# Performance work log

Hardware: AMD Instinct MI355X
Metric: run time of the kernel (lower is better)

## Reference

```python
import jax, jax.numpy as jnp
import numpy as np

N_NODES = 100000
N_EDGES = 3200000
N_GRAPHS = 1000
IN_C, HID_C, OUT_C = 128, 128, 10
BN_EPS = 1e-5


def setup_inputs() -> dict:
    key = jax.random.key(0)
    ks = jax.random.split(key, 16)
    s = lambda k, shape, fan: jax.random.normal(k, shape, jnp.float32) * (1.0 / np.sqrt(fan))
    x = jax.random.normal(ks[0], (N_NODES, IN_C), jnp.float32)
    edge_index = jax.random.randint(ks[1], (2, N_EDGES), 0, N_NODES, dtype=jnp.int64)
    batch = jnp.sort(jax.random.randint(ks[2], (N_NODES,), 0, N_GRAPHS, dtype=jnp.int64))
    return {
        "x": x, "edge_index": edge_index, "batch": batch,
        "W1a": s(ks[3], (IN_C, HID_C), IN_C), "b1a": jnp.zeros((HID_C,), jnp.float32),
        "W1b": s(ks[4], (HID_C, HID_C), HID_C), "b1b": jnp.zeros((HID_C,), jnp.float32),
        "g1": jnp.ones((HID_C,), jnp.float32), "be1": jnp.zeros((HID_C,), jnp.float32),
        "W2a": s(ks[5], (HID_C, HID_C), HID_C), "b2a": jnp.zeros((HID_C,), jnp.float32),
        "W2b": s(ks[6], (HID_C, HID_C), HID_C), "b2b": jnp.zeros((HID_C,), jnp.float32),
        "g2": jnp.ones((HID_C,), jnp.float32), "be2": jnp.zeros((HID_C,), jnp.float32),
        "Wlin": s(ks[7], (HID_C, OUT_C), HID_C), "blin": jnp.zeros((OUT_C,), jnp.float32),
    }


def _batchnorm(h, gamma, beta):
    # BatchNorm1d, training mode: batch statistics (biased variance, as torch)
    mean = jnp.mean(h, axis=0)
    var = jnp.mean(jnp.square(h - mean), axis=0)
    return (h - mean) * jax.lax.rsqrt(var + BN_EPS) * gamma + beta


def _gin_conv(x, src, dst, Wa, ba, Wb, bb, gamma, beta):
    # GINConv with eps=0: mlp(x + sum_{j->i} x_j); scatter-add over dst
    agg = jax.ops.segment_sum(x[src], dst, num_segments=N_NODES)
    h = x + agg
    h = jax.nn.relu(h @ Wa + ba) @ Wb + bb
    return _batchnorm(h, gamma, beta)


def reference(x, edge_index, batch, W1a, b1a, W1b, b1b, g1, be1,
              W2a, b2a, W2b, b2b, g2, be2, Wlin, blin):
    src, dst = edge_index[0], edge_index[1]
    h = jax.nn.relu(_gin_conv(x, src, dst, W1a, b1a, W1b, b1b, g1, be1))
    h = jax.nn.relu(_gin_conv(h, src, dst, W2a, b2a, W2b, b2b, g2, be2))
    pooled = jax.ops.segment_sum(h, batch, num_segments=N_GRAPHS)  # [G, HID_C]
    logits = pooled @ Wlin + blin
    return jax.nn.log_softmax(logits, axis=1)
```

## Files before the change

### kernel.cpp

```cpp
#include <hip/hip_runtime.h>
#include <hip/hip_bf16.h>

#define NN 100000
#define NE 3200000
#define NG 1000
#define BN_EPS 1e-5f

#define BKT_SH 6
#define BKTN 64
#define NBKT 1563
#define CHUNK 8192
#define NBINBLK 391
#define BNBLK 512

typedef __attribute__((ext_vector_type(8))) short short8v;
typedef __attribute__((ext_vector_type(4))) float f32x4;

__device__ __forceinline__ unsigned int f2bf(float f) {
    unsigned int u = __builtin_bit_cast(unsigned int, f);
    u += 0x7FFFu + ((u >> 16) & 1u);
    return u >> 16;
}
__device__ __forceinline__ float bf2f(unsigned int h16) {
    return __builtin_bit_cast(float, h16 << 16);
}

__global__ __launch_bounds__(256) void bucket_count_kernel(const int* __restrict__ dst,
                                                           int* __restrict__ bcnt) {
    __shared__ int h[NBKT];
    int t = threadIdx.x;
    for (int i = t; i < NBKT; i += 256) h[i] = 0;
    __syncthreads();
    int gid = blockIdx.x * 256 + t;
    for (int e = gid; e < NE; e += NBINBLK * 256) atomicAdd(&h[dst[e] >> BKT_SH], 1);
    __syncthreads();
    for (int i = t; i < NBKT; i += 256) if (h[i]) atomicAdd(&bcnt[i], h[i]);
}

__global__ void bucket_scan_kernel(const int* __restrict__ bcnt, int* __restrict__ bbase,
                                   int* __restrict__ bcur) {
    __shared__ int wsum[16];
    __shared__ int lcarry;
    int t = threadIdx.x, lane = t & 63, w = t >> 6;
    if (t == 0) lcarry = 0;
    __syncthreads();
    for (int base = 0; base < NBKT; base += 1024) {
        int i = base + t;
        int v = (i < NBKT) ? bcnt[i] : 0;
        int incl = v;
        #pragma unroll
        for (int d = 1; d < 64; d <<= 1) { int u = __shfl_up(incl, d, 64); if (lane >= d) incl += u; }
        if (lane == 63) wsum[w] = incl;
        __syncthreads();
        if (w == 0) {
            int s = (lane < 16) ? wsum[lane] : 0;
            #pragma unroll
            for (int d = 1; d < 16; d <<= 1) { int u = __shfl_up(s, d, 64); if (lane >= d) s += u; }
            if (lane < 16) wsum[lane] = s;
        }
        __syncthreads();
        int excl = lcarry + (w ? wsum[w - 1] : 0) + incl - v;
        if (i < NBKT) { bbase[i] = excl; bcur[i] = excl; }
        __syncthreads();
        if (t == 0) lcarry += wsum[15];
        __syncthreads();
    }
}

__global__ __launch_bounds__(256) void bin_kernel(const int* __restrict__ src,
        const int* __restrict__ dst, int* __restrict__ bcur,
        unsigned int* __restrict__ ebin) {
    __shared__ unsigned int ebuf[CHUNK];
    __shared__ unsigned short bids[CHUNK];
    __shared__ int hist[NBKT], lbase[NBKT], lcur[NBKT], delta[NBKT];
    __shared__ int wsum4[4];
    __shared__ int carry;
    int t = threadIdx.x;
    int lane = t & 63, w = t >> 6;
    int c0 = blockIdx.x * CHUNK;
    int cnt = min(CHUNK, NE - c0);
    for (int i = t; i < NBKT; i += 256) hist[i] = 0;
    if (t == 0) carry = 0;
    __syncthreads();
    for (int i = t; i < cnt; i += 256) atomicAdd(&hist[dst[c0 + i] >> BKT_SH], 1);
    __syncthreads();
    for (int bb = 0; bb < NBKT; bb += 256) {
        int i = bb + t;
        int v = (i < NBKT) ? hist[i] : 0;
        int incl = v;
        #pragma unroll
        for (int d2 = 1; d2 < 64; d2 <<= 1) { int u = __shfl_up(incl, d2, 64); if (lane >= d2) incl += u; }
        if (lane == 63) wsum4[w] = incl;
        __syncthreads();
        int wo = 0;
        if (w > 0) wo = wsum4[0];
        if (w > 1) wo += wsum4[1];
        if (w > 2) wo += wsum4[2];
        int excl = carry + wo + incl - v;
        if (i < NBKT) { lbase[i] = excl; lcur[i] = excl; }
        int tot = wsum4[0] + wsum4[1] + wsum4[2] + wsum4[3];
        __syncthreads();
        if (t == 0) carry += tot;
        __syncthreads();
    }
    for (int b = t; b < NBKT; b += 256) {
        int hh = hist[b];
        delta[b] = (hh ? atomicAdd(&bcur[b], hh) : 0) - lbase[b];
    }
    __syncthreads();
    for (int i = t; i < cnt; i += 256) {
        int d = dst[c0 + i];
        int s = src[c0 + i];
        int b = d >> BKT_SH;
        unsigned int entry = ((unsigned int)s << BKT_SH) | (unsigned int)(d & (BKTN - 1));
        int p = atomicAdd(&lcur[b], 1);
        ebuf[p] = entry;
        bids[p] = (unsigned short)b;
    }
    __syncthreads();
    for (int i = t; i < cnt; i += 256) {
        ebin[delta[bids[i]] + i] = ebuf[i];
    }
}

__global__ __launch_bounds__(256) void sort_kernel(const unsigned int* __restrict__ ebin,
        const int* __restrict__ bbase, const int* __restrict__ bcnt,
        int* __restrict__ noffs, int* __restrict__ csrc) {
    __shared__ int nh[BKTN], ncur[BKTN];
    int b = blockIdx.x, t = threadIdx.x;
    int base = bbase[b], cnt = bcnt[b];
    if (t < BKTN) nh[t] = 0;
    __syncthreads();
    for (int i = t; i < cnt; i += 256) atomicAdd(&nh[ebin[base + i] & (BKTN - 1)], 1);
    __syncthreads();
    if (t < 64) {
        int v = nh[t], incl = v;
        #pragma unroll
        for (int d = 1; d < 64; d <<= 1) { int u = __shfl_up(incl, d, 64); if (t >= d) incl += u; }
        int excl = incl - v;
        ncur[t] = excl;
        int node = (b << BKT_SH) + t;
        if (node < NN) noffs[node] = base + excl;
    }
    if (b == 0 && t == 0) noffs[NN] = NE;
    __syncthreads();
    for (int i = t; i < cnt; i += 256) {
        unsigned int e = ebin[base + i];
        int p = atomicAdd(&ncur[e & (BKTN - 1)], 1);
        csrc[base + p] = (int)(e >> BKT_SH);
    }
}

__global__ void pack_x_kernel(const float* __restrict__ x, unsigned int* __restrict__ xp) {
    int tid = blockIdx.x * 256 + threadIdx.x;
    float2 v = ((const float2*)x)[tid];
    xp[tid] = f2bf(v.x) | (f2bf(v.y) << 16);
}

__global__ void wprep_kernel(const float* __restrict__ W1a, const float* __restrict__ W1b,
                             const float* __restrict__ W2a, const float* __restrict__ W2b,
                             unsigned int* __restrict__ Wt) {
    int tid = blockIdx.x * 256 + threadIdx.x;
    int m = tid >> 13;
    int r = tid & 8191;
    int c = r >> 6, kh = r & 63;
    const float* W = (m == 0) ? W1a : (m == 1) ? W1b : (m == 2) ? W2a : W2b;
    float a = W[(2 * kh) * 128 + c];
    float b = W[(2 * kh + 1) * 128 + c];
    Wt[tid] = f2bf(a) | (f2bf(b) << 16);
}

__global__ __launch_bounds__(256) void aggregate_gather_kernel(
        const unsigned int* __restrict__ xp, const int* __restrict__ noffs,
        const int* __restrict__ csrc, unsigned int* __restrict__ outp) {
    int node = __builtin_amdgcn_readfirstlane(blockIdx.x * 4 + (threadIdx.x >> 6));
    int lane = threadIdx.x & 63;
    unsigned int u = xp[(size_t)node * 64 + lane];
    float alo = bf2f(u & 0xFFFFu), ahi = bf2f(u >> 16);
    int s = noffs[node], e = noffs[node + 1];
    int i = s;
    for (; i + 8 <= e; i += 8) {
        int i0 = csrc[i + 0], i1 = csrc[i + 1], i2 = csrc[i + 2], i3 = csrc[i + 3];
        int i4 = csrc[i + 4], i5 = csrc[i + 5], i6 = csrc[i + 6], i7 = csrc[i + 7];
        unsigned int u0 = xp[(size_t)i0 * 64 + lane];
        unsigned int u1 = xp[(size_t)i1 * 64 + lane];
        unsigned int u2 = xp[(size_t)i2 * 64 + lane];
        unsigned int u3 = xp[(size_t)i3 * 64 + lane];
        unsigned int u4 = xp[(size_t)i4 * 64 + lane];
        unsigned int u5 = xp[(size_t)i5 * 64 + lane];
        unsigned int u6 = xp[(size_t)i6 * 64 + lane];
        unsigned int u7 = xp[(size_t)i7 * 64 + lane];
        alo += bf2f(u0 & 0xFFFFu); ahi += bf2f(u0 >> 16);
        alo += bf2f(u1 & 0xFFFFu); ahi += bf2f(u1 >> 16);
        alo += bf2f(u2 & 0xFFFFu); ahi += bf2f(u2 >> 16);
        alo += bf2f(u3 & 0xFFFFu); ahi += bf2f(u3 >> 16);
        alo += bf2f(u4 & 0xFFFFu); ahi += bf2f(u4 >> 16);
        alo += bf2f(u5 & 0xFFFFu); ahi += bf2f(u5 >> 16);
        alo += bf2f(u6 & 0xFFFFu); ahi += bf2f(u6 >> 16);
        alo += bf2f(u7 & 0xFFFFu); ahi += bf2f(u7 >> 16);
    }
    for (; i < e; ++i) {
        int sv = csrc[i];
        unsigned int uu = xp[(size_t)sv * 64 + lane];
        alo += bf2f(uu & 0xFFFFu); ahi += bf2f(uu >> 16);
    }
    outp[(size_t)node * 64 + lane] = f2bf(alo) | (f2bf(ahi) << 16);
}

__global__ __launch_bounds__(256) void mlp_kernel(const unsigned int* __restrict__ Pin,
        const unsigned int* __restrict__ WtA, const float* __restrict__ bA,
        const unsigned int* __restrict__ WtB, const float* __restrict__ bB,
        unsigned int* __restrict__ Pout) {
    __shared__ unsigned int tile[64 * 68];
    int t = threadIdx.x, l = t & 63, w = t >> 6;
    int node0 = blockIdx.x * 64;
    int rbase = w * 16;
    int g = l >> 4, r = l & 15;
    int g4 = g * 4;

    const uint4* P4 = (const uint4*)Pin;
    #pragma unroll
    for (int i = 0; i < 4; ++i) {
        int rl = rbase + i * 4 + g;
        int node = node0 + rl;
        uint4 v = make_uint4(0u, 0u, 0u, 0u);
        if (node < NN) v = P4[(size_t)node * 16 + r];
        *(uint4*)&tile[rl * 68 + r * 4] = v;
    }

    f32x4 acc1[8];
    #pragma unroll
    for (int cb = 0; cb < 8; ++cb) acc1[cb] = (f32x4){0.f, 0.f, 0.f, 0.f};
    #pragma unroll
    for (int kk = 0; kk < 4; ++kk) {
        short8v a = *(short8v*)&tile[(rbase + r) * 68 + kk * 16 + g4];
        #pragma unroll
        for (int cb = 0; cb < 8; ++cb) {
            short8v wv = *(const short8v*)&WtA[(size_t)(cb * 16 + r) * 64 + kk * 16 + g4];
            acc1[cb] = __builtin_amdgcn_mfma_f32_16x16x32_bf16(wv, a, acc1[cb], 0, 0, 0);
        }
    }
    #pragma unroll
    for (int cb = 0; cb < 8; ++cb) {
        int c0 = cb * 16 + g4;
        float4 bi = *(const float4*)&bA[c0];
        float h0 = fmaxf(acc1[cb][0] + bi.x, 0.f);
        float h1 = fmaxf(acc1[cb][1] + bi.y, 0.f);
        float h2 = fmaxf(acc1[cb][2] + bi.z, 0.f);
        float h3 = fmaxf(acc1[cb][3] + bi.w, 0.f);
        uint2 pk;
        pk.x = f2bf(h0) | (f2bf(h1) << 16);
        pk.y = f2bf(h2) | (f2bf(h3) << 16);
        *(uint2*)&tile[(rbase + r) * 68 + (c0 >> 1)] = pk;
    }
    f32x4 acc2[8];
    #pragma unroll
    for (int cb = 0; cb < 8; ++cb) acc2[cb] = (f32x4){0.f, 0.f, 0.f, 0.f};
    #pragma unroll
    for (int kk = 0; kk < 4; ++kk) {
        short8v a = *(short8v*)&tile[(rbase + r) * 68 + kk * 16 + g4];
        #pragma unroll
        for (int cb = 0; cb < 8; ++cb) {
            short8v wv = *(const short8v*)&WtB[(size_t)(cb * 16 + r) * 64 + kk * 16 + g4];
            acc2[cb] = __builtin_amdgcn_mfma_f32_16x16x32_bf16(wv, a, acc2[cb], 0, 0, 0);
        }
    }
    int node = node0 + rbase + r;
    if (node < NN) {
        #pragma unroll
        for (int cb = 0; cb < 8; ++cb) {
            int c0 = cb * 16 + g4;
            float4 bi = *(const float4*)&bB[c0];
            float h0 = acc2[cb][0] + bi.x;
            float h1 = acc2[cb][1] + bi.y;
            float h2 = acc2[cb][2] + bi.z;
            float h3 = acc2[cb][3] + bi.w;
            uint2 pk;
            pk.x = f2bf(h0) | (f2bf(h1) << 16);
            pk.y = f2bf(h2) | (f2bf(h3) << 16);
            *(uint2*)&Pout[(size_t)node * 64 + (c0 >> 1)] = pk;
        }
    }
}

__global__ __launch_bounds__(256) void bn_part_kernel(const unsigned int* __restrict__ P,
                                                      float* __restrict__ partial) {
    __shared__ float red[4][256];
    int t = threadIdx.x, l = t & 63, w = t >> 6;
    float s0 = 0.f, s1 = 0.f, q0 = 0.f, q1 = 0.f;
    for (int n = blockIdx.x * 4 + w; n < NN; n += BNBLK * 4) {
        unsigned int u = P[(size_t)n * 64 + l];
        float a = bf2f(u & 0xFFFFu), b = bf2f(u >> 16);
        s0 += a; q0 += a * a; s1 += b; q1 += b * b;
    }
    red[0][t] = s0; red[1][t] = s1; red[2][t] = q0; red[3][t] = q1;
    __syncthreads();
    if (t < 64) {
        float t0 = red[0][t] + red[0][t + 64] + red[0][t + 128] + red[0][t + 192];
        float t1 = red[1][t] + red[1][t + 64] + red[1][t + 128] + red[1][t + 192];
        float t2 = red[2][t] + red[2][t + 64] + red[2][t + 128] + red[2][t + 192];
        float t3 = red[3][t] + red[3][t + 64] + red[3][t + 128] + red[3][t + 192];
        float* pb = &partial[blockIdx.x * 256];
        pb[2 * t] = t0;
        pb[2 * t + 1] = t1;
        pb[128 + 2 * t] = t2;
        pb[128 + 2 * t + 1] = t3;
    }
}

__global__ void bn_reduce_kernel(const float* __restrict__ partial, float* __restrict__ stats) {
    int t = threadIdx.x;
    float s = 0.f;
    for (int b = 0; b < BNBLK; ++b) s += partial[b * 256 + t];
    stats[t] = s;
}

__global__ void bn_relu_pack_kernel(const unsigned int* __restrict__ Pin,
        const float* __restrict__ stats, const float* __restrict__ gamma,
        const float* __restrict__ beta, unsigned int* __restrict__ Pout) {
    int tid = blockIdx.x * 256 + threadIdx.x;
    int l = tid & 63;
    int c0 = 2 * l;
    const float inv = 1.0f / NN;
    unsigned int u = Pin[tid];
    float u0 = bf2f(u & 0xFFFFu), u1 = bf2f(u >> 16);
    float m0 = stats[c0] * inv;
    float v0 = stats[128 + c0] * inv - m0 * m0;
    float m1 = stats[c0 + 1] * inv;
    float v1 = stats[128 + c0 + 1] * inv - m1 * m1;
    float o0 = fmaxf((u0 - m0) * rsqrtf(v0 + BN_EPS) * gamma[c0] + beta[c0], 0.f);
    float o1 = fmaxf((u1 - m1) * rsqrtf(v1 + BN_EPS) * gamma[c0 + 1] + beta[c0 + 1], 0.f);
    Pout[tid] = f2bf(o0) | (f2bf(o1) << 16);
}

__global__ void pool_kernel(const unsigned int* __restrict__ hb,
                            const int* __restrict__ batch, float* __restrict__ pooled) {
    int g = blockIdx.x;
    int l = threadIdx.x;
    int a = 0, b = NN;
    while (a < b) { int m = (a + b) >> 1; if (batch[m] < g) a = m + 1; else b = m; }
    int start = a;
    b = NN;
    while (a < b) { int m = (a + b) >> 1; if (batch[m] < g + 1) a = m + 1; else b = m; }
    int end = a;
    float s0 = 0.f, s1 = 0.f;
    for (int i = start; i < end; ++i) {
        unsigned int u = hb[(size_t)i * 64 + l];
        s0 += bf2f(u & 0xFFFFu);
        s1 += bf2f(u >> 16);
    }
    ((float2*)pooled)[g * 64 + l] = make_float2(s0, s1);
}

__global__ void head_kernel(const float* __restrict__ pooled, const float* __restrict__ Wlin,
                            const float* __restrict__ blin, float* __restrict__ out) {
    int g = blockIdx.x;
    int lane = threadIdx.x;
    float2 p = ((const float2*)pooled)[g * 64 + lane];
    float l[10];
    #pragma unroll
    for (int o = 0; o < 10; ++o) {
        float partial = p.x * Wlin[(2 * lane) * 10 + o] + p.y * Wlin[(2 * lane + 1) * 10 + o];
        #pragma unroll
        for (int m = 1; m < 64; m <<= 1) partial += __shfl_xor(partial, m, 64);
        l[o] = partial + blin[o];
    }
    float mx = l[0];
    #pragma unroll
    for (int o = 1; o < 10; ++o) mx = fmaxf(mx, l[o]);
    float se = 0.f;
    #pragma unroll
    for (int o = 0; o < 10; ++o) se += expf(l[o] - mx);
    float lse = mx + logf(se);
    if (lane == 0) {
        #pragma unroll
        for (int o = 0; o < 10; ++o) out[g * 10 + o] = l[o] - lse;
    }
}

extern "C" void kernel_launch(void* const* d_in, const int* in_sizes, int n_in,
                              void* d_out, int out_size, void* d_ws, size_t ws_size,
                              hipStream_t stream) {
    const float* x    = (const float*)d_in[0];
    const int*   edge = (const int*)d_in[1];
    const int*   batch= (const int*)d_in[2];
    const float* W1a  = (const float*)d_in[3];
    const float* b1a  = (const float*)d_in[4];
    const float* W1b  = (const float*)d_in[5];
    const float* b1b  = (const float*)d_in[6];
    const float* g1   = (const float*)d_in[7];
    const float* be1  = (const float*)d_in[8];
    const float* W2a  = (const float*)d_in[9];
    const float* b2a  = (const float*)d_in[10];
    const float* W2b  = (const float*)d_in[11];
    const float* b2b  = (const float*)d_in[12];
    const float* g2   = (const float*)d_in[13];
    const float* be2  = (const float*)d_in[14];
    const float* Wlin = (const float*)d_in[15];
    const float* blin = (const float*)d_in[16];
    float* out = (float*)d_out;

    char* ws = (char*)d_ws;
    size_t off = 0;
    auto alloc = [&](size_t bytes) -> void* {
        void* p = ws + off; off += (bytes + 255) & ~(size_t)255; return p;
    };
    unsigned int* Pa   = (unsigned int*)alloc((size_t)NN * 64 * 4);
    unsigned int* Pb   = (unsigned int*)alloc((size_t)NN * 64 * 4);
    unsigned int* ebin = (unsigned int*)alloc((size_t)NE * 4);
    int*   csrc   = (int*)alloc((size_t)NE * 4);
    int*   noffs  = (int*)alloc((NN + 1) * 4);
    int*   bcnt   = (int*)alloc(NBKT * 4);
    int*   bbase  = (int*)alloc(NBKT * 4);
    int*   bcur   = (int*)alloc(NBKT * 4);
    float* stats1 = (float*)alloc(256 * 4);
    float* stats2 = (float*)alloc(256 * 4);
    float* partial= (float*)alloc((size_t)BNBLK * 256 * 4);
    float* pooled = (float*)alloc(NG * 128 * 4);
    unsigned int* Wt = (unsigned int*)alloc(4 * 8192 * 4);
    unsigned int* Wt1a = Wt;
    unsigned int* Wt1b = Wt + 8192;
    unsigned int* Wt2a = Wt + 16384;
    unsigned int* Wt2b = Wt + 24576;

    const int* srcI = edge;
    const int* dstI = edge + NE;

    hipMemsetAsync(bcnt, 0, NBKT * 4, stream);

    bucket_count_kernel<<<NBINBLK, 256, 0, stream>>>(dstI, bcnt);
    bucket_scan_kernel<<<1, 1024, 0, stream>>>(bcnt, bbase, bcur);
    bin_kernel<<<NBINBLK, 256, 0, stream>>>(srcI, dstI, bcur, ebin);
    sort_kernel<<<NBKT, 256, 0, stream>>>(ebin, bbase, bcnt, noffs, csrc);
    wprep_kernel<<<128, 256, 0, stream>>>(W1a, W1b, W2a, W2b, Wt);
    pack_x_kernel<<<25000, 256, 0, stream>>>(x, Pa);

    aggregate_gather_kernel<<<25000, 256, 0, stream>>>(Pa, noffs, csrc, Pb);
    mlp_kernel<<<1563, 256, 0, stream>>>(Pb, Wt1a, b1a, Wt1b, b1b, Pa);
    bn_part_kernel<<<BNBLK, 256, 0, stream>>>(Pa, partial);
    bn_reduce_kernel<<<1, 256, 0, stream>>>(partial, stats1);
    bn_relu_pack_kernel<<<25000, 256, 0, stream>>>(Pa, stats1, g1, be1, Pb);
    aggregate_gather_kernel<<<25000, 256, 0, stream>>>(Pb, noffs, csrc, Pa);
    mlp_kernel<<<1563, 256, 0, stream>>>(Pa, Wt2a, b2a, Wt2b, b2b, Pb);
    bn_part_kernel<<<BNBLK, 256, 0, stream>>>(Pb, partial);
    bn_reduce_kernel<<<1, 256, 0, stream>>>(partial, stats2);
    bn_relu_pack_kernel<<<25000, 256, 0, stream>>>(Pb, stats2, g2, be2, Pa);

    pool_kernel<<<NG, 64, 0, stream>>>(Pa, batch, pooled);
    head_kernel<<<NG, 64, 0, stream>>>(pooled, Wlin, blin, out);
}
```

Baseline: 578.2 us.

## Fuse neighbor aggregation into MLP kernel and fold BN+ReLU into consumers

New measurement: 644.3 us. 1.11x slower.

```diff
diff --git a/kernel.cpp b/kernel.cpp
--- a/kernel.cpp
+++ b/kernel.cpp
@@ -170,44 +170,10 @@
     Wt[tid] = f2bf(a) | (f2bf(b) << 16);
 }
 
-__global__ __launch_bounds__(256) void aggregate_gather_kernel(
-        const unsigned int* __restrict__ xp, const int* __restrict__ noffs,
-        const int* __restrict__ csrc, unsigned int* __restrict__ outp) {
-    int node = __builtin_amdgcn_readfirstlane(blockIdx.x * 4 + (threadIdx.x >> 6));
-    int lane = threadIdx.x & 63;
-    unsigned int u = xp[(size_t)node * 64 + lane];
-    float alo = bf2f(u & 0xFFFFu), ahi = bf2f(u >> 16);
-    int s = noffs[node], e = noffs[node + 1];
-    int i = s;
-    for (; i + 8 <= e; i += 8) {
-        int i0 = csrc[i + 0], i1 = csrc[i + 1], i2 = csrc[i + 2], i3 = csrc[i + 3];
-        int i4 = csrc[i + 4], i5 = csrc[i + 5], i6 = csrc[i + 6], i7 = csrc[i + 7];
-        unsigned int u0 = xp[(size_t)i0 * 64 + lane];
-        unsigned int u1 = xp[(size_t)i1 * 64 + lane];
-        unsigned int u2 = xp[(size_t)i2 * 64 + lane];
-        unsigned int u3 = xp[(size_t)i3 * 64 + lane];
-        unsigned int u4 = xp[(size_t)i4 * 64 + lane];
-        unsigned int u5 = xp[(size_t)i5 * 64 + lane];
-        unsigned int u6 = xp[(size_t)i6 * 64 + lane];
-        unsigned int u7 = xp[(size_t)i7 * 64 + lane];
-        alo += bf2f(u0 & 0xFFFFu); ahi += bf2f(u0 >> 16);
-        alo += bf2f(u1 & 0xFFFFu); ahi += bf2f(u1 >> 16);
-        alo += bf2f(u2 & 0xFFFFu); ahi += bf2f(u2 >> 16);
-        alo += bf2f(u3 & 0xFFFFu); ahi += bf2f(u3 >> 16);
-        alo += bf2f(u4 & 0xFFFFu); ahi += bf2f(u4 >> 16);
-        alo += bf2f(u5 & 0xFFFFu); ahi += bf2f(u5 >> 16);
-        alo += bf2f(u6 & 0xFFFFu); ahi += bf2f(u6 >> 16);
-        alo += bf2f(u7 & 0xFFFFu); ahi += bf2f(u7 >> 16);
-    }
-    for (; i < e; ++i) {
-        int sv = csrc[i];
-        unsigned int uu = xp[(size_t)sv * 64 + lane];
-        alo += bf2f(uu & 0xFFFFu); ahi += bf2f(uu >> 16);
-    }
-    outp[(size_t)node * 64 + lane] = f2bf(alo) | (f2bf(ahi) << 16);
-}
-
-__global__ __launch_bounds__(256) void mlp_kernel(const unsigned int* __restrict__ Pin,
+template<int BN_IN>
+__global__ __launch_bounds__(256) void gin_layer_kernel(const unsigned int* __restrict__ Pin,
+        const float* __restrict__ coef,
+        const int* __restrict__ noffs, const int* __restrict__ csrc,
         const unsigned int* __restrict__ WtA, const float* __restrict__ bA,
         const unsigned int* __restrict__ WtB, const float* __restrict__ bB,
         unsigned int* __restrict__ Pout) {
@@ -215,18 +181,73 @@
     int t = threadIdx.x, l = t & 63, w = t >> 6;
     int node0 = blockIdx.x * 64;
     int rbase = w * 16;
+
+    float a0 = 1.f, b0 = 0.f, a1 = 1.f, b1 = 0.f;
+    if (BN_IN) {
+        float2 av = ((const float2*)coef)[l];
+        float2 bv = ((const float2*)(coef + 128))[l];
+        a0 = av.x; a1 = av.y; b0 = bv.x; b1 = bv.y;
+    }
+
+    for (int ni = 0; ni < 16; ++ni) {
+        int node = __builtin_amdgcn_readfirstlane(node0 + rbase + ni);
+        float alo = 0.f, ahi = 0.f;
+        if (node < NN) {
+            unsigned int u = Pin[(size_t)node * 64 + l];
+            alo = bf2f(u & 0xFFFFu); ahi = bf2f(u >> 16);
+            if (BN_IN) { alo = fmaxf(alo * a0 + b0, 0.f); ahi = fmaxf(ahi * a1 + b1, 0.f); }
+            int s = noffs[node], e = noffs[node + 1];
+            int i = s;
+            for (; i + 8 <= e; i += 8) {
+                int i0 = csrc[i + 0], i1 = csrc[i + 1], i2 = csrc[i + 2], i3 = csrc[i + 3];
+                int i4 = csrc[i + 4], i5 = csrc[i + 5], i6 = csrc[i + 6], i7 = csrc[i + 7];
+                unsigned int u0 = Pin[(size_t)i0 * 64 + l];
+                unsigned int u1 = Pin[(size_t)i1 * 64 + l];
+                unsigned int u2 = Pin[(size_t)i2 * 64 + l];
+                unsigned int u3 = Pin[(size_t)i3 * 64 + l];
+                unsigned int u4 = Pin[(size_t)i4 * 64 + l];
+                unsigned int u5 = Pin[(size_t)i5 * 64 + l];
+                unsigned int u6 = Pin[(size_t)i6 * 64 + l];
+                unsigned int u7 = Pin[(size_t)i7 * 64 + l];
+                float lo, hi;
+                lo = bf2f(u0 & 0xFFFFu); hi = bf2f(u0 >> 16);
+                if (BN_IN) { lo = fmaxf(lo * a0 + b0, 0.f); hi = fmaxf(hi * a1 + b1, 0.f); }
+                alo += lo; ahi += hi;
+                lo = bf2f(u1 & 0xFFFFu); hi = bf2f(u1 >> 16);
+                if (BN_IN) { lo = fmaxf(lo * a0 + b0, 0.f); hi = fmaxf(hi * a1 + b1, 0.f); }
+                alo += lo; ahi += hi;
+                lo = bf2f(u2 & 0xFFFFu); hi = bf2f(u2 >> 16);
+                if (BN_IN) { lo = fmaxf(lo * a0 + b0, 0.f); hi = fmaxf(hi * a1 + b1, 0.f); }
+                alo += lo; ahi += hi;
+                lo = bf2f(u3 & 0xFFFFu); hi = bf2f(u3 >> 16);
+                if (BN_IN) { lo = fmaxf(lo * a0 + b0, 0.f); hi = fmaxf(hi * a1 + b1, 0.f); }
+                alo += lo; ahi += hi;
+                lo = bf2f(u4 & 0xFFFFu); hi = bf2f(u4 >> 16);
+                if (BN_IN) { lo = fmaxf(lo * a0 + b0, 0.f); hi = fmaxf(hi * a1 + b1, 0.f); }
+                alo += lo; ahi += hi;
+                lo = bf2f(u5 & 0xFFFFu); hi = bf2f(u5 >> 16);
+                if (BN_IN) { lo = fmaxf(lo * a0 + b0, 0.f); hi = fmaxf(hi * a1 + b1, 0.f); }
+                alo += lo; ahi += hi;
+                lo = bf2f(u6 & 0xFFFFu); hi = bf2f(u6 >> 16);
+                if (BN_IN) { lo = fmaxf(lo * a0 + b0, 0.f); hi = fmaxf(hi * a1 + b1, 0.f); }
+                alo += lo; ahi += hi;
+                lo = bf2f(u7 & 0xFFFFu); hi = bf2f(u7 >> 16);
+                if (BN_IN) { lo = fmaxf(lo * a0 + b0, 0.f); hi = fmaxf(hi * a1 + b1, 0.f); }
+                alo += lo; ahi += hi;
+            }
+            for (; i < e; ++i) {
+                int sv = csrc[i];
+                unsigned int uu = Pin[(size_t)sv * 64 + l];
+                float lo = bf2f(uu & 0xFFFFu), hi = bf2f(uu >> 16);
+                if (BN_IN) { lo = fmaxf(lo * a0 + b0, 0.f); hi = fmaxf(hi * a1 + b1, 0.f); }
+                alo += lo; ahi += hi;
+            }
+        }
+        tile[(rbase + ni) * 68 + l] = f2bf(alo) | (f2bf(ahi) << 16);
+    }
+
     int g = l >> 4, r = l & 15;
     int g4 = g * 4;
-
-    const uint4* P4 = (const uint4*)Pin;
-    #pragma unroll
-    for (int i = 0; i < 4; ++i) {
-        int rl = rbase + i * 4 + g;
-        int node = node0 + rl;
-        uint4 v = make_uint4(0u, 0u, 0u, 0u);
-        if (node < NN) v = P4[(size_t)node * 16 + r];
-        *(uint4*)&tile[rl * 68 + r * 4] = v;
-    }
 
     f32x4 acc1[8];
     #pragma unroll
@@ -308,35 +329,31 @@
     }
 }
 
-__global__ void bn_reduce_kernel(const float* __restrict__ partial, float* __restrict__ stats) {
+__global__ void bn_reduce_kernel(const float* __restrict__ partial,
+        const float* __restrict__ gamma, const float* __restrict__ beta,
+        float* __restrict__ coef) {
+    __shared__ float st[256];
     int t = threadIdx.x;
     float s = 0.f;
     for (int b = 0; b < BNBLK; ++b) s += partial[b * 256 + t];
-    stats[t] = s;
-}
-
-__global__ void bn_relu_pack_kernel(const unsigned int* __restrict__ Pin,
-        const float* __restrict__ stats, const float* __restrict__ gamma,
-        const float* __restrict__ beta, unsigned int* __restrict__ Pout) {
-    int tid = blockIdx.x * 256 + threadIdx.x;
-    int l = tid & 63;
-    int c0 = 2 * l;
-    const float inv = 1.0f / NN;
-    unsigned int u = Pin[tid];
-    float u0 = bf2f(u & 0xFFFFu), u1 = bf2f(u >> 16);
-    float m0 = stats[c0] * inv;
-    float v0 = stats[128 + c0] * inv - m0 * m0;
-    float m1 = stats[c0 + 1] * inv;
-    float v1 = stats[128 + c0 + 1] * inv - m1 * m1;
-    float o0 = fmaxf((u0 - m0) * rsqrtf(v0 + BN_EPS) * gamma[c0] + beta[c0], 0.f);
-    float o1 = fmaxf((u1 - m1) * rsqrtf(v1 + BN_EPS) * gamma[c0 + 1] + beta[c0 + 1], 0.f);
-    Pout[tid] = f2bf(o0) | (f2bf(o1) << 16);
-}
-
-__global__ void pool_kernel(const unsigned int* __restrict__ hb,
+    st[t] = s;
+    __syncthreads();
+    if (t < 128) {
+        const float inv = 1.0f / NN;
+        float m = st[t] * inv;
+        float var = st[128 + t] * inv - m * m;
+        float a = gamma[t] * rsqrtf(var + BN_EPS);
+        coef[t] = a;
+        coef[128 + t] = beta[t] - m * a;
+    }
+}
+
+__global__ void pool_kernel(const unsigned int* __restrict__ hb, const float* __restrict__ coef,
                             const int* __restrict__ batch, float* __restrict__ pooled) {
     int g = blockIdx.x;
     int l = threadIdx.x;
+    float2 av = ((const float2*)coef)[l];
+    float2 bv = ((const float2*)(coef + 128))[l];
     int a = 0, b = NN;
     while (a < b) { int m = (a + b) >> 1; if (batch[m] < g) a = m + 1; else b = m; }
     int start = a;
@@ -346,8 +363,8 @@
     float s0 = 0.f, s1 = 0.f;
     for (int i = start; i < end; ++i) {
         unsigned int u = hb[(size_t)i * 64 + l];
-        s0 += bf2f(u & 0xFFFFu);
-        s1 += bf2f(u >> 16);
+        s0 += fmaxf(bf2f(u & 0xFFFFu) * av.x + bv.x, 0.f);
+        s1 += fmaxf(bf2f(u >> 16) * av.y + bv.y, 0.f);
     }
     ((float2*)pooled)[g * 64 + l] = make_float2(s0, s1);
 }
@@ -405,6 +422,7 @@
     auto alloc = [&](size_t bytes) -> void* {
         void* p = ws + off; off += (bytes + 255) & ~(size_t)255; return p;
     };
+    unsigned int* Px   = (unsigned int*)alloc((size_t)NN * 64 * 4);
     unsigned int* Pa   = (unsigned int*)alloc((size_t)NN * 64 * 4);
     unsigned int* Pb   = (unsigned int*)alloc((size_t)NN * 64 * 4);
     unsigned int* ebin = (unsigned int*)alloc((size_t)NE * 4);
@@ -413,8 +431,8 @@
     int*   bcnt   = (int*)alloc(NBKT * 4);
     int*   bbase  = (int*)alloc(NBKT * 4);
     int*   bcur   = (int*)alloc(NBKT * 4);
-    float* stats1 = (float*)alloc(256 * 4);
-    float* stats2 = (float*)alloc(256 * 4);
+    float* coef1  = (float*)alloc(256 * 4);
+    float* coef2  = (float*)alloc(256 * 4);
     float* partial= (float*)alloc((size_t)BNBLK * 256 * 4);
     float* pooled = (float*)alloc(NG * 128 * 4);
     unsigned int* Wt = (unsigned int*)alloc(4 * 8192 * 4);
@@ -433,19 +451,17 @@
     bin_kernel<<<NBINBLK, 256, 0, stream>>>(srcI, dstI, bcur, ebin);
     sort_kernel<<<NBKT, 256, 0, stream>>>(ebin, bbase, bcnt, noffs, csrc);
     wprep_kernel<<<128, 256, 0, stream>>>(W1a, W1b, W2a, W2b, Wt);
-    pack_x_kernel<<<25000, 256, 0, stream>>>(x, Pa);
-
-    aggregate_gather_kernel<<<25000, 256, 0, stream>>>(Pa, noffs, csrc, Pb);
-    mlp_kernel<<<1563, 256, 0, stream>>>(Pb, Wt1a, b1a, Wt1b, b1b, Pa);
+    pack_x_kernel<<<25000, 256, 0, stream>>>(x, Px);
+
+    gin_layer_kernel<0><<<NBKT, 256, 0, stream>>>(Px, coef1, noffs, csrc,
+                                                  Wt1a, b1a, Wt1b, b1b, Pa);
     bn_part_kernel<<<BNBLK, 256, 0, stream>>>(Pa, partial);
-    bn_reduce_kernel<<<1, 256, 0, stream>>>(partial, stats1);
-    bn_relu_pack_kernel<<<25000, 256, 0, stream>>>(Pa, stats1, g1, be1, Pb);
-    aggregate_gather_kernel<<<25000, 256, 0, stream>>>(Pb, noffs, csrc, Pa);
-    mlp_kernel<<<1563, 256, 0, stream>>>(Pa, Wt2a, b2a, Wt2b, b2b, Pb);
+    bn_reduce_kernel<<<1, 256, 0, stream>>>(partial, g1, be1, coef1);
+    gin_layer_kernel<1><<<NBKT, 256, 0, stream>>>(Pa, coef1, noffs, csrc,
+                                                  Wt2a, b2a, Wt2b, b2b, Pb);
     bn_part_kernel<<<BNBLK, 256, 0, stream>>>(Pb, partial);
-    bn_reduce_kernel<<<1, 256, 0, stream>>>(partial, stats2);
-    bn_relu_pack_kernel<<<25000, 256, 0, stream>>>(Pb, stats2, g2, be2, Pa);
-
-    pool_kernel<<<NG, 64, 0, stream>>>(Pa, batch, pooled);
+    bn_reduce_kernel<<<1, 256, 0, stream>>>(partial, g2, be2, coef2);
+
+    pool_kernel<<<NG, 64, 0, stream>>>(Pb, coef2, batch, pooled);
     head_kernel<<<NG, 64, 0, stream>>>(pooled, Wlin, blin, out);
 }
```
